# Optimization experiments

Hardware: AMD Instinct MI355X
Metric: run time of the kernel (lower is better)

## Reference

```python
import jax, jax.numpy as jnp
import numpy as np

N = 50000   # nodes
E = 800000  # edges (avg degree 16)
D = 128     # hidden_channels
L = 4       # num_layers
ALPHA = 0.1


def setup_inputs() -> dict:
    key = jax.random.key(0)
    ks = jax.random.split(key, 6)
    x = jax.random.normal(ks[0], (N, D), dtype=jnp.float32)
    w = jax.random.uniform(ks[1], (E,), dtype=jnp.float32)
    src = jax.random.randint(ks[2], (E,), 0, N)
    dst = jax.random.randint(ks[3], (E,), 0, N)
    # stacked per-layer Linear params
    W = jax.random.normal(ks[4], (L, D, D), dtype=jnp.float32) / np.float32(np.sqrt(D))
    b = jax.random.normal(ks[5], (L, D), dtype=jnp.float32) * 0.01
    # GPR coefficients: alpha*(1-alpha)^k, last = (1-alpha)^L
    temp_np = ALPHA * (1 - ALPHA) ** np.arange(L + 1)
    temp_np[-1] = (1 - ALPHA) ** L
    temp = jnp.asarray(temp_np, dtype=jnp.float32)
    return {"x": x, "w": w, "src": src, "dst": dst, "W": W, "b": b, "temp": temp}


def reference(x, w, src, dst, W, b, temp):
    # eval mode: dropout / dropout_adj are no-ops; edge_attn=False
    hidden = x * temp[0]
    for i in range(L):
        h = x @ W[i] + b[i]                 # [N, D] linear
        msg = h[src] * w[:, None]           # gather + edge-weight, [E, D]
        x = jax.ops.segment_sum(msg, dst, num_segments=N)  # scatter-sum
        x = jax.nn.relu(x)
        hidden = hidden + x * temp[i + 1]
    return hidden
```

## Files before the change

kernel.cpp:

```cpp
#include <hip/hip_runtime.h>
#include <hip/hip_fp16.h>

#define N_NODES 50000
#define N_EDGES 800000
#define DIM 128
#define LAYERS 4
#define SLOT 48
#define EPB 8

#define BUCKET_BLOCKS 3128
#define WT_BLOCKS 256
#define INIT_BLOCKS 3125

typedef __attribute__((ext_vector_type(8))) _Float16 half8;
typedef __attribute__((ext_vector_type(4))) float float4v;
typedef __attribute__((ext_vector_type(2))) float float2v;

__device__ __forceinline__ int pack_edge(int s, float w) {
    return (int)(((unsigned)__half_as_ushort(__float2half(w)) << 16) | (unsigned)(s & 0xFFFF));
}

__device__ __forceinline__ void fp8x8_to_f32(uint2 v, float* f) {
    float2v a = __builtin_amdgcn_cvt_pk_f32_fp8(v.x, false);
    float2v b = __builtin_amdgcn_cvt_pk_f32_fp8(v.x, true);
    float2v c = __builtin_amdgcn_cvt_pk_f32_fp8(v.y, false);
    float2v d = __builtin_amdgcn_cvt_pk_f32_fp8(v.y, true);
    f[0] = a[0]; f[1] = a[1]; f[2] = b[0]; f[3] = b[1];
    f[4] = c[0]; f[5] = c[1]; f[6] = d[0]; f[7] = d[1];
}

__device__ __forceinline__ uint2 f32x8_to_fp8(const float* f) {
    unsigned lo = 0, hi = 0;
    lo = __builtin_amdgcn_cvt_pk_fp8_f32(f[0], f[1], lo, false);
    lo = __builtin_amdgcn_cvt_pk_fp8_f32(f[2], f[3], lo, true);
    hi = __builtin_amdgcn_cvt_pk_fp8_f32(f[4], f[5], hi, false);
    hi = __builtin_amdgcn_cvt_pk_fp8_f32(f[6], f[7], hi, true);
    return make_uint2(lo, hi);
}

__device__ __forceinline__ void bucket_one(int d, int s, float wv, int g,
                                           int* __restrict__ cnt,
                                           int* __restrict__ edge_buf) {
    if ((d & 7) == g) {
        int pos = atomicAdd(&cnt[d], 1);
        edge_buf[(size_t)d * SLOT + pos] = pack_edge(s, wv);
    }
}

__global__ __launch_bounds__(256) void prep_kernel(const int* __restrict__ src,
                                                   const int* __restrict__ dst,
                                                   const float* __restrict__ w,
                                                   int* __restrict__ cnt,
                                                   int* __restrict__ edge_buf,
                                                   const float* __restrict__ W,
                                                   __half* __restrict__ Wt,
                                                   const float4* __restrict__ x,
                                                   uint2* __restrict__ xh0) {
    int bid = blockIdx.x;
    int tid = threadIdx.x;
    if (bid < BUCKET_BLOCKS) {
        int g     = bid & 7;
        int chunk = bid >> 3;
        int base  = (chunk * 256 + tid) * EPB;
        if (base >= N_EDGES) return;
        int4   d4a = *(const int4*)(dst + base);
        int4   d4b = *(const int4*)(dst + base + 4);
        int4   s4a = *(const int4*)(src + base);
        int4   s4b = *(const int4*)(src + base + 4);
        float4 w4a = *(const float4*)(w + base);
        float4 w4b = *(const float4*)(w + base + 4);
        bucket_one(d4a.x, s4a.x, w4a.x, g, cnt, edge_buf);
        bucket_one(d4a.y, s4a.y, w4a.y, g, cnt, edge_buf);
        bucket_one(d4a.z, s4a.z, w4a.z, g, cnt, edge_buf);
        bucket_one(d4a.w, s4a.w, w4a.w, g, cnt, edge_buf);
        bucket_one(d4b.x, s4b.x, w4b.x, g, cnt, edge_buf);
        bucket_one(d4b.y, s4b.y, w4b.y, g, cnt, edge_buf);
        bucket_one(d4b.z, s4b.z, w4b.z, g, cnt, edge_buf);
        bucket_one(d4b.w, s4b.w, w4b.w, g, cnt, edge_buf);
    } else if (bid < BUCKET_BLOCKS + WT_BLOCKS) {
        int i = (bid - BUCKET_BLOCKS) * 256 + tid;
        int l   = i >> 14;
        int rem = i & 16383;
        int k = rem >> 7;
        int n = rem & 127;
        Wt[(size_t)l * DIM * DIM + n * DIM + k] =
            __float2half(W[(size_t)l * DIM * DIM + k * DIM + n]);
    } else {
        int i = (bid - BUCKET_BLOCKS - WT_BLOCKS) * 256 + tid;
        float4 a = x[(size_t)i * 2];
        float4 b = x[(size_t)i * 2 + 1];
        float f[8] = { a.x, a.y, a.z, a.w, b.x, b.y, b.z, b.w };
        xh0[i] = f32x8_to_fp8(f);
    }
}

__device__ __forceinline__ void batch8(const uint2* __restrict__ x8,
                                       int m, int base, int cnt_r, int r, int c,
                                       float* accf, float& wsum) {
    uint2 v[8]; float wv[8];
    #pragma unroll
    for (int u = 0; u < 8; ++u) {
        int jj = base + u;
        int p  = __shfl(m, (r << 4) | (jj & 15), 64);
        bool live = (jj < cnt_r);
        wv[u] = live
                  ? __half2float(__ushort_as_half((unsigned short)((unsigned)p >> 16)))
                  : 0.f;
        uint2 vv = make_uint2(0u, 0u);
        if (live) vv = x8[(size_t)(p & 0xFFFF) * 16 + c];
        v[u] = vv;
    }
    #pragma unroll
    for (int u = 0; u < 8; ++u) {
        wsum += wv[u];
        float f[8];
        fp8x8_to_f32(v[u], f);
        #pragma unroll
        for (int t = 0; t < 8; ++t)
            accf[t] += wv[u] * f[t];
    }
}

#define AP 136
template <bool FINAL>
__global__ __launch_bounds__(256) void layer_kernel(const uint2* __restrict__ xin8,
                                                    const int* __restrict__ cnt_arr,
                                                    const int* __restrict__ edge_buf,
                                                    const __half* __restrict__ Wt,
                                                    const float* __restrict__ bl,
                                                    uint2* __restrict__ xout,
                                                    float* __restrict__ hidden,
                                                    const float* __restrict__ temp,
                                                    const uint2* __restrict__ x0h,
                                                    const uint2* __restrict__ x1h,
                                                    const uint2* __restrict__ x2h) {
    __shared__ __half Ah[16][AP];
    __shared__ float winS[16];
    int tid  = threadIdx.x;
    int wave = tid >> 6;
    int lane = tid & 63;
    int r = lane >> 4;
    int c = lane & 15;
    int node0  = blockIdx.x * 16 + wave * 4;
    int node_r = node0 + r;

    size_t mb = (size_t)node_r * SLOT;
    int m0 = edge_buf[mb + c];
    int m1 = edge_buf[mb + 16 + c];
    int4 c4 = *(const int4*)(cnt_arr + node0);

    int cnt_r = (r == 0) ? c4.x : (r == 1) ? c4.y : (r == 2) ? c4.z : c4.w;
    int maxc  = max(max(c4.x, c4.y), max(c4.z, c4.w));

    float accf[8];
    #pragma unroll
    for (int t = 0; t < 8; ++t) accf[t] = 0.f;
    float wsum = 0.f;

    batch8(xin8, m0, 0, cnt_r, r, c, accf, wsum);
    batch8(xin8, m0, 8, cnt_r, r, c, accf, wsum);
    if (maxc > 16) {
        batch8(xin8, m1, 16, cnt_r, r, c, accf, wsum);
        batch8(xin8, m1, 24, cnt_r, r, c, accf, wsum);
    }
    if (maxc > 32) {
        int m2 = edge_buf[mb + 32 + c];
        batch8(xin8, m2, 32, cnt_r, r, c, accf, wsum);
        batch8(xin8, m2, 40, cnt_r, r, c, accf, wsum);
    }

    union { __half2 hh[4]; float4 f4; } ua;
    ua.hh[0] = __floats2half2_rn(accf[0], accf[1]);
    ua.hh[1] = __floats2half2_rn(accf[2], accf[3]);
    ua.hh[2] = __floats2half2_rn(accf[4], accf[5]);
    ua.hh[3] = __floats2half2_rn(accf[6], accf[7]);
    int lr = wave * 4 + r;
    *(float4*)&Ah[lr][c * 8] = ua.f4;
    if (c == 0) winS[lr] = wsum;
    __syncthreads();

    int am  = lane & 15;
    int ak8 = (lane >> 4) * 8;
    float4v acc0 = (float4v)(0.f), acc1 = (float4v)(0.f);
    #pragma unroll
    for (int kk = 0; kk < 4; ++kk) {
        int k0 = kk * 32 + ak8;
        half8 a  = *(const half8*)&Ah[am][k0];
        half8 b0 = *(const half8*)(Wt + (size_t)(wave * 32 + am) * DIM + k0);
        half8 b1 = *(const half8*)(Wt + (size_t)(wave * 32 + 16 + am) * DIM + k0);
        acc0 = __builtin_amdgcn_mfma_f32_16x16x32_f16(a, b0, acc0, 0, 0, 0);
        acc1 = __builtin_amdgcn_mfma_f32_16x16x32_f16(a, b1, acc1, 0, 0, 0);
    }
    __syncthreads();

    int q  = lane >> 4;
    int cc = lane & 15;
    {
        int col = wave * 32 + cc;
        float bv = bl[col];
        #pragma unroll
        for (int j = 0; j < 4; ++j) {
            int row = q * 4 + j;
            Ah[row][col] = __float2half(fmaxf(acc0[j] + winS[row] * bv, 0.f));
        }
        col = wave * 32 + 16 + cc;
        bv = bl[col];
        #pragma unroll
        for (int j = 0; j < 4; ++j) {
            int row = q * 4 + j;
            Ah[row][col] = __float2half(fmaxf(acc1[j] + winS[row] * bv, 0.f));
        }
    }
    __syncthreads();

    int row = tid >> 4;
    int ch  = tid & 15;
    int gnode = blockIdx.x * 16 + row;
    half8 hv = *(const half8*)&Ah[row][ch * 8];
    size_t ro = (size_t)gnode * 16 + ch;

    if constexpr (!FINAL) {
        float f[8];
        #pragma unroll
        for (int t = 0; t < 8; ++t) f[t] = (float)hv[t];
        xout[ro] = f32x8_to_fp8(f);
    } else {
        float t0 = temp[0], t1 = temp[1], t2 = temp[2], t3 = temp[3], t4 = temp[4];
        uint2 u0 = x0h[ro], u1 = x1h[ro], u2 = x2h[ro], u3 = xin8[ro];
        float f0[8], f1[8], f2[8], f3[8];
        fp8x8_to_f32(u0, f0);
        fp8x8_to_f32(u1, f1);
        fp8x8_to_f32(u2, f2);
        fp8x8_to_f32(u3, f3);
        float out[8];
        #pragma unroll
        for (int t = 0; t < 8; ++t)
            out[t] = t0 * f0[t] + t1 * f1[t] + t2 * f2[t]
                   + t3 * f3[t] + t4 * (float)hv[t];
        size_t o = (size_t)gnode * DIM + ch * 8;
        *(float4*)(hidden + o)     = make_float4(out[0], out[1], out[2], out[3]);
        *(float4*)(hidden + o + 4) = make_float4(out[4], out[5], out[6], out[7]);
    }
}

extern "C" void kernel_launch(void* const* d_in, const int* in_sizes, int n_in,
                              void* d_out, int out_size, void* d_ws, size_t ws_size,
                              hipStream_t stream) {
    const float* x    = (const float*)d_in[0];
    const float* w    = (const float*)d_in[1];
    const int*   src  = (const int*)d_in[2];
    const int*   dst  = (const int*)d_in[3];
    const float* W    = (const float*)d_in[4];
    const float* b    = (const float*)d_in[5];
    const float* temp = (const float*)d_in[6];
    float* hidden = (float*)d_out;

    char* ws = (char*)d_ws;
    uint2* X0 = (uint2*)ws;                  ws += (size_t)N_NODES * DIM;
    uint2* X1 = (uint2*)ws;                  ws += (size_t)N_NODES * DIM;
    uint2* X2 = (uint2*)ws;                  ws += (size_t)N_NODES * DIM;
    uint2* X3 = (uint2*)ws;                  ws += (size_t)N_NODES * DIM;
    __half* Wt = (__half*)ws;                ws += (size_t)LAYERS * DIM * DIM * sizeof(__half);
    int* cnt = (int*)ws;                     ws += (size_t)N_NODES * sizeof(int);
    int* edge_buf = (int*)ws;                ws += (size_t)(N_NODES * SLOT + 64) * sizeof(int);

    hipMemsetAsync(cnt, 0, (size_t)N_NODES * sizeof(int), stream);
    prep_kernel<<<BUCKET_BLOCKS + WT_BLOCKS + INIT_BLOCKS, 256, 0, stream>>>(
        src, dst, w, cnt, edge_buf, W, Wt, (const float4*)x, X0);

    const int layer_blocks = N_NODES / 16;
    layer_kernel<false><<<layer_blocks, 256, 0, stream>>>(
        X0, cnt, edge_buf, Wt + 0 * DIM * DIM, b + 0 * DIM,
        X1, hidden, temp, nullptr, nullptr, nullptr);
    layer_kernel<false><<<layer_blocks, 256, 0, stream>>>(
        X1, cnt, edge_buf, Wt + 1 * DIM * DIM, b + 1 * DIM,
        X2, hidden, temp, nullptr, nullptr, nullptr);
    layer_kernel<false><<<layer_blocks, 256, 0, stream>>>(
        X2, cnt, edge_buf, Wt + 2 * DIM * DIM, b + 2 * DIM,
        X3, hidden, temp, nullptr, nullptr, nullptr);
    layer_kernel<true><<<layer_blocks, 256, 0, stream>>>(
        X3, cnt, edge_buf, Wt + 3 * DIM * DIM, b + 3 * DIM,
        nullptr, hidden, temp, X0, X1, X2);
}
```

Baseline: 247.5 us.

## Split fused layer kernel into separate gather and matmul kernels per layer

New measurement: 287.4 us. 16.1% more time.

```diff
diff --git a/kernel.cpp b/kernel.cpp
--- a/kernel.cpp
+++ b/kernel.cpp
@@ -11,6 +11,10 @@
 #define BUCKET_BLOCKS 3128
 #define WT_BLOCKS 256
 #define INIT_BLOCKS 3125
+
+#define GTILES 1563
+#define G_BLOCKS 3128
+#define M_BLOCKS 3125
 
 typedef __attribute__((ext_vector_type(8))) _Float16 half8;
 typedef __attribute__((ext_vector_type(4))) float float4v;
@@ -94,20 +98,19 @@
     }
 }
 
-__device__ __forceinline__ void batch8(const uint2* __restrict__ x8,
-                                       int m, int base, int cnt_r, int r, int c,
-                                       float* accf, float& wsum) {
+__device__ __forceinline__ void batch8h(const uint2* __restrict__ x8,
+                                        int m, int base, int cnt_r, int sgb, int hc,
+                                        float* accf, float& wsum) {
     uint2 v[8]; float wv[8];
     #pragma unroll
     for (int u = 0; u < 8; ++u) {
-        int jj = base + u;
-        int p  = __shfl(m, (r << 4) | (jj & 15), 64);
-        bool live = (jj < cnt_r);
+        int p = __shfl(m, sgb | u, 64);
+        bool live = (base + u) < cnt_r;
         wv[u] = live
                   ? __half2float(__ushort_as_half((unsigned short)((unsigned)p >> 16)))
                   : 0.f;
         uint2 vv = make_uint2(0u, 0u);
-        if (live) vv = x8[(size_t)(p & 0xFFFF) * 16 + c];
+        if (live) vv = x8[(size_t)(p & 0xFFFF) * 16 + hc];
         v[u] = vv;
     }
     #pragma unroll
@@ -121,62 +124,90 @@
     }
 }
 
+__global__ __launch_bounds__(256) void gather_kernel(const uint2* __restrict__ xin8,
+                                                     const int* __restrict__ cnt_arr,
+                                                     const int* __restrict__ edge_buf,
+                                                     __half* __restrict__ A,
+                                                     float* __restrict__ wsumg) {
+    int q = blockIdx.x >> 3, rr = blockIdx.x & 7;
+    int half = rr >> 2;
+    int tile = q * 4 + (rr & 3);
+    if (tile >= GTILES) return;
+    int tid  = threadIdx.x;
+    int wave = tid >> 6;
+    int lane = tid & 63;
+    int sg  = lane >> 3;
+    int c   = lane & 7;
+    int sgb = lane & 0x38;
+    int node_r = tile * 32 + wave * 8 + sg;
+    bool valid = node_r < N_NODES;
+    size_t mb = (size_t)(valid ? node_r : 0) * SLOT;
+    int m0a = edge_buf[mb + c];
+    int m0b = edge_buf[mb + 8 + c];
+    int m1a = edge_buf[mb + 16 + c];
+    int m1b = edge_buf[mb + 24 + c];
+    int cnt_r = valid ? cnt_arr[node_r] : 0;
+    int maxc = cnt_r;
+    maxc = max(maxc, __shfl_xor(maxc, 8, 64));
+    maxc = max(maxc, __shfl_xor(maxc, 16, 64));
+    maxc = max(maxc, __shfl_xor(maxc, 32, 64));
+
+    int hc = half * 8 + c;
+    float accf[8];
+    #pragma unroll
+    for (int t = 0; t < 8; ++t) accf[t] = 0.f;
+    float wsum = 0.f;
+
+    batch8h(xin8, m0a, 0, cnt_r, sgb, hc, accf, wsum);
+    batch8h(xin8, m0b, 8, cnt_r, sgb, hc, accf, wsum);
+    if (maxc > 16) {
+        batch8h(xin8, m1a, 16, cnt_r, sgb, hc, accf, wsum);
+        batch8h(xin8, m1b, 24, cnt_r, sgb, hc, accf, wsum);
+    }
+    if (maxc > 32) {
+        int m2a = edge_buf[mb + 32 + c];
+        int m2b = edge_buf[mb + 40 + c];
+        batch8h(xin8, m2a, 32, cnt_r, sgb, hc, accf, wsum);
+        batch8h(xin8, m2b, 40, cnt_r, sgb, hc, accf, wsum);
+    }
+
+    if (valid) {
+        union { __half2 hh[4]; float4 f4; } ua;
+        ua.hh[0] = __floats2half2_rn(accf[0], accf[1]);
+        ua.hh[1] = __floats2half2_rn(accf[2], accf[3]);
+        ua.hh[2] = __floats2half2_rn(accf[4], accf[5]);
+        ua.hh[3] = __floats2half2_rn(accf[6], accf[7]);
+        *(float4*)(A + (size_t)node_r * DIM + half * 64 + c * 8) = ua.f4;
+        if (half == 0 && c == 0) wsumg[node_r] = wsum;
+    }
+}
+
 #define AP 136
 template <bool FINAL>
-__global__ __launch_bounds__(256) void layer_kernel(const uint2* __restrict__ xin8,
-                                                    const int* __restrict__ cnt_arr,
-                                                    const int* __restrict__ edge_buf,
-                                                    const __half* __restrict__ Wt,
-                                                    const float* __restrict__ bl,
-                                                    uint2* __restrict__ xout,
-                                                    float* __restrict__ hidden,
-                                                    const float* __restrict__ temp,
-                                                    const uint2* __restrict__ x0h,
-                                                    const uint2* __restrict__ x1h,
-                                                    const uint2* __restrict__ x2h) {
+__global__ __launch_bounds__(256) void mm_kernel(const __half* __restrict__ A,
+                                                 const float* __restrict__ wsumg,
+                                                 const __half* __restrict__ Wt,
+                                                 const float* __restrict__ bl,
+                                                 uint2* __restrict__ xout,
+                                                 float* __restrict__ hidden,
+                                                 const float* __restrict__ temp,
+                                                 const uint2* __restrict__ x0h,
+                                                 const uint2* __restrict__ x1h,
+                                                 const uint2* __restrict__ x2h,
+                                                 const uint2* __restrict__ x3h) {
     __shared__ __half Ah[16][AP];
     __shared__ float winS[16];
     int tid  = threadIdx.x;
     int wave = tid >> 6;
     int lane = tid & 63;
-    int r = lane >> 4;
-    int c = lane & 15;
-    int node0  = blockIdx.x * 16 + wave * 4;
-    int node_r = node0 + r;
-
-    size_t mb = (size_t)node_r * SLOT;
-    int m0 = edge_buf[mb + c];
-    int m1 = edge_buf[mb + 16 + c];
-    int4 c4 = *(const int4*)(cnt_arr + node0);
-
-    int cnt_r = (r == 0) ? c4.x : (r == 1) ? c4.y : (r == 2) ? c4.z : c4.w;
-    int maxc  = max(max(c4.x, c4.y), max(c4.z, c4.w));
-
-    float accf[8];
-    #pragma unroll
-    for (int t = 0; t < 8; ++t) accf[t] = 0.f;
-    float wsum = 0.f;
-
-    batch8(xin8, m0, 0, cnt_r, r, c, accf, wsum);
-    batch8(xin8, m0, 8, cnt_r, r, c, accf, wsum);
-    if (maxc > 16) {
-        batch8(xin8, m1, 16, cnt_r, r, c, accf, wsum);
-        batch8(xin8, m1, 24, cnt_r, r, c, accf, wsum);
-    }
-    if (maxc > 32) {
-        int m2 = edge_buf[mb + 32 + c];
-        batch8(xin8, m2, 32, cnt_r, r, c, accf, wsum);
-        batch8(xin8, m2, 40, cnt_r, r, c, accf, wsum);
-    }
-
-    union { __half2 hh[4]; float4 f4; } ua;
-    ua.hh[0] = __floats2half2_rn(accf[0], accf[1]);
-    ua.hh[1] = __floats2half2_rn(accf[2], accf[3]);
-    ua.hh[2] = __floats2half2_rn(accf[4], accf[5]);
-    ua.hh[3] = __floats2half2_rn(accf[6], accf[7]);
-    int lr = wave * 4 + r;
-    *(float4*)&Ah[lr][c * 8] = ua.f4;
-    if (c == 0) winS[lr] = wsum;
+    int gnode0 = blockIdx.x * 16;
+
+    {
+        int row = tid >> 4, ch = tid & 15;
+        *(float4*)&Ah[row][ch * 8] =
+            *(const float4*)(A + (size_t)(gnode0 + row) * DIM + ch * 8);
+    }
+    if (tid < 16) winS[tid] = wsumg[gnode0 + tid];
     __syncthreads();
 
     int am  = lane & 15;
@@ -215,7 +246,7 @@
 
     int row = tid >> 4;
     int ch  = tid & 15;
-    int gnode = blockIdx.x * 16 + row;
+    int gnode = gnode0 + row;
     half8 hv = *(const half8*)&Ah[row][ch * 8];
     size_t ro = (size_t)gnode * 16 + ch;
 
@@ -226,7 +257,7 @@
         xout[ro] = f32x8_to_fp8(f);
     } else {
         float t0 = temp[0], t1 = temp[1], t2 = temp[2], t3 = temp[3], t4 = temp[4];
-        uint2 u0 = x0h[ro], u1 = x1h[ro], u2 = x2h[ro], u3 = xin8[ro];
+        uint2 u0 = x0h[ro], u1 = x1h[ro], u2 = x2h[ro], u3 = x3h[ro];
         float f0[8], f1[8], f2[8], f3[8];
         fp8x8_to_f32(u0, f0);
         fp8x8_to_f32(u1, f1);
@@ -263,22 +294,25 @@
     __half* Wt = (__half*)ws;                ws += (size_t)LAYERS * DIM * DIM * sizeof(__half);
     int* cnt = (int*)ws;                     ws += (size_t)N_NODES * sizeof(int);
     int* edge_buf = (int*)ws;                ws += (size_t)(N_NODES * SLOT + 64) * sizeof(int);
+    __half* A = (__half*)ws;                 ws += (size_t)N_NODES * DIM * sizeof(__half);
+    float* wsumg = (float*)ws;               ws += (size_t)N_NODES * sizeof(float);
 
     hipMemsetAsync(cnt, 0, (size_t)N_NODES * sizeof(int), stream);
     prep_kernel<<<BUCKET_BLOCKS + WT_BLOCKS + INIT_BLOCKS, 256, 0, stream>>>(
         src, dst, w, cnt, edge_buf, W, Wt, (const float4*)x, X0);
 
-    const int layer_blocks = N_NODES / 16;
-    layer_kernel<false><<<layer_blocks, 256, 0, stream>>>(
-        X0, cnt, edge_buf, Wt + 0 * DIM * DIM, b + 0 * DIM,
-        X1, hidden, temp, nullptr, nullptr, nullptr);
-    layer_kernel<false><<<layer_blocks, 256, 0, stream>>>(
-        X1, cnt, edge_buf, Wt + 1 * DIM * DIM, b + 1 * DIM,
-        X2, hidden, temp, nullptr, nullptr, nullptr);
-    layer_kernel<false><<<layer_blocks, 256, 0, stream>>>(
-        X2, cnt, edge_buf, Wt + 2 * DIM * DIM, b + 2 * DIM,
-        X3, hidden, temp, nullptr, nullptr, nullptr);
-    layer_kernel<true><<<layer_blocks, 256, 0, stream>>>(
-        X3, cnt, edge_buf, Wt + 3 * DIM * DIM, b + 3 * DIM,
-        nullptr, hidden, temp, X0, X1, X2);
-}
+    uint2* Xs[4] = { X0, X1, X2, X3 };
+    for (int l = 0; l < LAYERS; ++l) {
+        gather_kernel<<<G_BLOCKS, 256, 0, stream>>>(
+            Xs[l], cnt, edge_buf, A, wsumg);
+        if (l < LAYERS - 1) {
+            mm_kernel<false><<<M_BLOCKS, 256, 0, stream>>>(
+                A, wsumg, Wt + (size_t)l * DIM * DIM, b + (size_t)l * DIM,
+                Xs[l + 1], hidden, temp, nullptr, nullptr, nullptr, nullptr);
+        } else {
+            mm_kernel<true><<<M_BLOCKS, 256, 0, stream>>>(
+                A, wsumg, Wt + (size_t)l * DIM * DIM, b + (size_t)l * DIM,
+                nullptr, hidden, temp, X0, X1, X2, X3);
+        }
+    }
+}
```
